# Optimization experiments

Measured on AMD Instinct MI355X. Metric: run time of the kernel, lower is better.

Reference implementation:

```python
import jax, jax.numpy as jnp
import numpy as np

HW = 128  # BEV heatmap size hardcoded in the module

def conv2d(x, w, b, pad):
    y = jax.lax.conv_general_dilated(x, w, (1, 1), [(pad, pad), (pad, pad)],
                                     dimension_numbers=('NCHW', 'OIHW', 'NCHW'))
    return y + b[None, :, None, None]

def setup_inputs() -> dict:
    key = jax.random.key(0)
    ks = jax.random.split(key, 8)
    B, C, N = 4, 64, 4096
    middle_feat_lidar = jax.random.normal(ks[0], (B, C, HW, HW), dtype=jnp.float32)
    voxels_feat_radar = jax.random.normal(ks[1], (N, C), dtype=jnp.float32)
    rcoors = jax.random.randint(ks[2], (N, 4), 0, HW, dtype=jnp.int64)
    rcoors = rcoors.at[:, 0].set(rcoors[:, 0] % B)  # batch index in [0, B)
    rcs = jax.random.uniform(ks[3], (N,), dtype=jnp.float32) * 6.0
    gamma = jnp.array(1.0, dtype=jnp.float32)  # self.rcs_gamma
    # rcs_att: Conv2d(2, C, 1); compress: Conv2d(2C, C, 3, pad=1)
    att_w = jax.random.normal(ks[4], (C, 2, 1, 1), dtype=jnp.float32) * 0.5
    att_b = jnp.zeros((C,), dtype=jnp.float32)
    comp_w = jax.random.normal(ks[5], (C, 2 * C, 3, 3), dtype=jnp.float32) * (1.0 / np.sqrt(2 * C * 9))
    comp_b = jnp.zeros((C,), dtype=jnp.float32)
    return {"middle_feat_lidar": middle_feat_lidar, "voxels_feat_radar": voxels_feat_radar,
            "rcoors": rcoors, "batch_size": B, "rcs": rcs, "gamma": gamma,
            "att_w": att_w, "att_b": att_b, "comp_w": comp_w, "comp_b": comp_b}

def _draw_maps(rcoors, rcs, gamma, batch_size):
    # Vectorized CenterPoint-style gaussian scatter-max over all N points.
    true_rcs = jax.nn.relu(rcs)                      # (N,)
    r = jnp.floor(gamma * true_rcs + 1.0)            # int() truncation; radius >= 1
    sigma = (2.0 * r + 1.0) / 6.0                    # sigma = diameter / 6
    b = rcoors[:, 0]
    y = rcoors[:, 2].astype(jnp.float32)
    x = rcoors[:, 3].astype(jnp.float32)
    grid = jnp.arange(HW, dtype=jnp.float32)
    dy = grid[None, :] - y[:, None]                  # (N, HW) rows
    dx = grid[None, :] - x[:, None]                  # (N, HW) cols
    g = jnp.exp(-(dy[:, :, None] ** 2 + dx[:, None, :] ** 2)
                / (2.0 * sigma[:, None, None] ** 2))  # (N, HW, HW)
    eps = jnp.finfo(jnp.float32).eps
    g = jnp.where(g < eps, 0.0, g)                   # gaussian_2d eps cutoff (max is 1 at center)
    # truncate gaussian to its (2r+1) box, as the slicing in draw_heatmap_gaussian does
    box = (jnp.abs(dy[:, :, None]) <= r[:, None, None]) & (jnp.abs(dx[:, None, :]) <= r[:, None, None])
    g = jnp.where(box, g, 0.0)
    heatmap = jnp.maximum(jax.ops.segment_max(g, b, num_segments=batch_size), 0.0)          # (B,HW,HW)
    heatmap_feat = jnp.maximum(
        jax.ops.segment_max(g * true_rcs[:, None, None], b, num_segments=batch_size), 0.0)  # (B,HW,HW)
    return heatmap, heatmap_feat

def reference(middle_feat_lidar, voxels_feat_radar, rcoors, batch_size, rcs,
              gamma, att_w, att_b, comp_w, comp_b):
    heatmap, heatmap_feat = _draw_maps(rcoors, rcs, gamma, batch_size)
    hm2 = jnp.stack([heatmap, heatmap_feat], axis=1)        # (B,2,HW,HW)
    rcs_features = conv2d(hm2, att_w, att_b, pad=0)          # 1x1 conv
    fused = jnp.concatenate([middle_feat_lidar, rcs_features], axis=1)
    return conv2d(fused, comp_w, comp_b, pad=1)              # 3x3 conv
```

## Files before the change

kernel.cpp:

```cpp
#include <hip/hip_runtime.h>
#include <math.h>

#define HW 128
#define CCH 64

typedef unsigned short u16;
typedef __attribute__((ext_vector_type(8))) short bf16x8;
typedef __attribute__((ext_vector_type(4))) float f32x4;

static __device__ __forceinline__ u16 f2bf(float x) {
    unsigned int u = __float_as_uint(x);
    unsigned int r = (u + 0x7FFFu + ((u >> 16) & 1u)) >> 16;
    return (u16)r;
}

__global__ void prep_kernel(const float* __restrict__ comp_w,
                            const float* __restrict__ att_w,
                            const float* __restrict__ att_b,
                            const int* __restrict__ rcoors,
                            const float* __restrict__ rcs,
                            const float* __restrict__ gamma_p,
                            float* __restrict__ Hm, float* __restrict__ Fm,
                            u16* __restrict__ Wp, int N, int B) {
    __shared__ float part[27][8];
    __shared__ float W3[27];
    int blk = blockIdx.x, tid = threadIdx.x;
    if (blk < 64) {
        int co = blk;
        if (tid < 216) {
            int d = tid >> 3, s = tid & 7;
            int t = d / 3, a = d - t * 3;
            float sum = 0.f;
#pragma unroll
            for (int q = 0; q < 8; ++q) {
                int c2 = s * 8 + q;
                float ww = comp_w[((size_t)co * 128 + 64 + c2) * 9 + t];
                float av = (a == 0) ? att_w[c2 * 2 + 0]
                         : (a == 1) ? att_w[c2 * 2 + 1]
                                    : att_b[c2];
                sum = fmaf(ww, av, sum);
            }
            part[d][s] = sum;
        }
        __syncthreads();
        if (tid < 27) {
            float s = 0.f;
#pragma unroll
            for (int q = 0; q < 8; ++q) s += part[tid][q];
            W3[tid] = s;
        }
        __syncthreads();
        for (int k = tid; k < 672; k += 256) {
            int oct = k >> 3, j = k & 7;
            u16 v = 0;
            if (oct < 81) {
                int t = oct / 9, o = oct - t * 9;
                int ci = o * 8 + j;
                float w = 0.0f;
                if (ci < 64)      w = comp_w[((size_t)co * 128 + ci) * 9 + t];
                else if (ci < 67) w = W3[t * 3 + (ci - 64)];
                v = f2bf(w);
            }
            Wp[co * 672 + k] = v;
        }
    } else {
        int n = blk - 64;
        if (n >= N) return;
        int b  = rcoors[n * 4 + 0];
        int yi = rcoors[n * 4 + 2];
        int xi = rcoors[n * 4 + 3];
        if ((unsigned)b >= (unsigned)B) return;
        float tr = fmaxf(rcs[n], 0.0f);
        float r = floorf(gamma_p[0] * tr + 1.0f);
        float sigma = (2.0f * r + 1.0f) * (1.0f / 6.0f);
        float inv2s2 = 1.0f / (2.0f * sigma * sigma);
        int R = (int)r;
        int W = 2 * R + 1;
        int tot = W * W;
        for (int cell = tid; cell < tot; cell += 256) {
            int cy = cell / W;
            int cx = cell - cy * W;
            int iy = yi - R + cy;
            int ix = xi - R + cx;
            if ((unsigned)iy >= HW || (unsigned)ix >= HW) continue;
            float dy = (float)(iy - yi), dx = (float)(ix - xi);
            float g = expf(-(dy * dy + dx * dx) * inv2s2);
            if (g < 1.1920929e-7f) continue;
            int idx = (b * HW + iy) * HW + ix;
            atomicMax((int*)&Hm[idx], __float_as_int(g));
            float gf = g * tr;
            if (gf > 0.0f) atomicMax((int*)&Fm[idx], __float_as_int(gf));
        }
    }
}

__global__ __launch_bounds__(256)
void conv_kernel(const float* __restrict__ middle,
                 const float* __restrict__ Hm, const float* __restrict__ Fm,
                 const u16* __restrict__ Wp, const float* __restrict__ comp_b,
                 float* __restrict__ out) {
    const int bx = blockIdx.x, by = blockIdx.y, b = blockIdx.z;
    const int tid = threadIdx.x;
    const int wave = tid >> 6, lane = tid & 63;
    const int col = lane & 15, quad = lane >> 4;
    const int i0 = by * 16 - 1, j0 = bx * 16 - 1;

    __shared__ u16 Xs[18 * 18 * 72];

    {
        const float* midB = middle + (size_t)b * CCH * HW * HW;
        const float* HmB = Hm + b * HW * HW;
        const float* FmB = Fm + b * HW * HW;
#pragma unroll 1
        for (int k0 = 0; k0 < 12; k0 += 6) {
            float rb[6][8];
#pragma unroll
            for (int q = 0; q < 6; ++q) {
                int u = tid + (k0 + q) * 256;
                int oct = u / 324, site = u - oct * 324;
                int rr = site / 18, cc = site - rr * 18;
                int gi = i0 + rr, gj = j0 + cc;
                bool in = (u < 2916) && ((unsigned)gi < HW) && ((unsigned)gj < HW);
                int off = in ? (gi * HW + gj) : 0;
                if (oct < 8) {
                    const float* p = midB + (size_t)(in ? oct : 0) * 8 * HW * HW + off;
#pragma unroll
                    for (int j = 0; j < 8; ++j)
                        rb[q][j] = p[(size_t)j * HW * HW];
                } else {
                    rb[q][0] = HmB[off];
                    rb[q][1] = FmB[off];
                }
            }
#pragma unroll
            for (int q = 0; q < 6; ++q) {
                int u = tid + (k0 + q) * 256;
                if (u >= 2916) continue;
                int oct = u / 324, site = u - oct * 324;
                int rr = site / 18, cc = site - rr * 18;
                int gi = i0 + rr, gj = j0 + cc;
                bool in = ((unsigned)gi < HW) && ((unsigned)gj < HW);
                union { u16 h[8]; uint4 v; } pk;
                pk.v = make_uint4(0u, 0u, 0u, 0u);
                if (in) {
                    if (oct < 8) {
#pragma unroll
                        for (int j = 0; j < 8; ++j) pk.h[j] = f2bf(rb[q][j]);
                    } else {
                        pk.h[0] = f2bf(rb[q][0]);
                        pk.h[1] = f2bf(rb[q][1]);
                        pk.h[2] = 0x3F80u;
                    }
                }
                *(uint4*)(Xs + site * 72 + oct * 8) = pk.v;
            }
        }
    }
    __syncthreads();

    f32x4 acc[4][4];
#pragma unroll
    for (int m = 0; m < 4; ++m)
#pragma unroll
        for (int n = 0; n < 4; ++n) acc[m][n] = (f32x4){0.f, 0.f, 0.f, 0.f};

#pragma unroll
    for (int c = 0; c < 21; ++c) {
        bf16x8 af[4];
#pragma unroll
        for (int m = 0; m < 4; ++m)
            af[m] = *(const bf16x8*)(Wp + (m * 16 + col) * 672 + c * 32 + quad * 8);

        int oct = c * 4 + quad;
        if (oct > 80) oct = 80;
        int t  = oct / 9;
        int o  = oct - t * 9;
        int dy = t / 3, dx = t - dy * 3;
        const u16* Bb = Xs + ((wave * 4 + dy) * 18 + (col + dx)) * 72 + o * 8;

        bf16x8 bfr[4];
#pragma unroll
        for (int n = 0; n < 4; ++n)
            bfr[n] = *(const bf16x8*)(Bb + n * (18 * 72));

#pragma unroll
        for (int m = 0; m < 4; ++m)
#pragma unroll
            for (int n = 0; n < 4; ++n)
                acc[m][n] = __builtin_amdgcn_mfma_f32_16x16x32_bf16(af[m], bfr[n], acc[m][n], 0, 0, 0);
    }

#pragma unroll
    for (int m = 0; m < 4; ++m) {
        int co0 = m * 16 + quad * 4;
#pragma unroll
        for (int n = 0; n < 4; ++n) {
            int i = by * 16 + wave * 4 + n;
            int j = bx * 16 + col;
            float* o0 = out + (((size_t)(b * 64 + co0) * HW + i) * HW + j);
#pragma unroll
            for (int r = 0; r < 4; ++r)
                o0[(size_t)r * HW * HW] = acc[m][n][r] + comp_b[co0 + r];
        }
    }
}

extern "C" void kernel_launch(void* const* d_in, const int* in_sizes, int n_in,
                              void* d_out, int out_size, void* d_ws, size_t ws_size,
                              hipStream_t stream) {
    const float* middle  = (const float*)d_in[0];
    const int*   rcoors  = (const int*)d_in[2];
    const float* rcs     = (const float*)d_in[4];
    const float* gamma   = (const float*)d_in[5];
    const float* att_w   = (const float*)d_in[6];
    const float* att_b   = (const float*)d_in[7];
    const float* comp_w  = (const float*)d_in[8];
    const float* comp_b  = (const float*)d_in[9];
    float* out = (float*)d_out;

    int B = in_sizes[0] / (CCH * HW * HW);
    int N = in_sizes[4];

    float* Hm = (float*)d_ws;
    float* Fm = Hm + (size_t)B * HW * HW;
    u16*   Wp = (u16*)(Fm + (size_t)B * HW * HW);

    prep_kernel<<<dim3(64 + N), 256, 0, stream>>>(comp_w, att_w, att_b,
                                                  rcoors, rcs, gamma,
                                                  Hm, Fm, Wp, N, B);
    conv_kernel<<<dim3(8, 8, B), 256, 0, stream>>>(middle, Hm, Fm, Wp, comp_b, out);
}
```

Baseline: 104.9 us.

## Shrink conv tile to 4x16 and split output channels across waves

The conv kernel now has each block compute a 4-row by 16-column output tile instead of 16x16, and each wave handles 16 output channels instead of 4 rows. The grid grows from 256 to 1024 blocks, which fills more CUs on the large GPU, and shared memory per block drops sharply, allowing higher occupancy. The cost is more halo reloading: 6 input rows are staged per 4 output rows instead of 18 per 16, which raises global read traffic on the 64-channel input. Per-wave MFMA register use also drops.

```diff
diff --git a/kernel.cpp b/kernel.cpp
--- a/kernel.cpp
+++ b/kernel.cpp
@@ -103,104 +103,90 @@
     const int tid = threadIdx.x;
     const int wave = tid >> 6, lane = tid & 63;
     const int col = lane & 15, quad = lane >> 4;
-    const int i0 = by * 16 - 1, j0 = bx * 16 - 1;
-
-    __shared__ u16 Xs[18 * 18 * 72];
+    const int i0 = by * 4 - 1, j0 = bx * 16 - 1;
+
+    __shared__ u16 Xs[6 * 18 * 72];
 
     {
         const float* midB = middle + (size_t)b * CCH * HW * HW;
         const float* HmB = Hm + b * HW * HW;
         const float* FmB = Fm + b * HW * HW;
-#pragma unroll 1
-        for (int k0 = 0; k0 < 12; k0 += 6) {
-            float rb[6][8];
-#pragma unroll
-            for (int q = 0; q < 6; ++q) {
-                int u = tid + (k0 + q) * 256;
-                int oct = u / 324, site = u - oct * 324;
-                int rr = site / 18, cc = site - rr * 18;
-                int gi = i0 + rr, gj = j0 + cc;
-                bool in = (u < 2916) && ((unsigned)gi < HW) && ((unsigned)gj < HW);
-                int off = in ? (gi * HW + gj) : 0;
+        float rb[4][8];
+#pragma unroll
+        for (int q = 0; q < 4; ++q) {
+            int u = tid + q * 256;
+            int oct = u / 108, site = u - oct * 108;
+            int rr = site / 18, cc = site - rr * 18;
+            int gi = i0 + rr, gj = j0 + cc;
+            bool in = (u < 972) && ((unsigned)gi < HW) && ((unsigned)gj < HW);
+            int off = in ? (gi * HW + gj) : 0;
+            if (oct < 8) {
+                const float* p = midB + (size_t)(in ? oct : 0) * 8 * HW * HW + off;
+#pragma unroll
+                for (int j = 0; j < 8; ++j)
+                    rb[q][j] = p[(size_t)j * HW * HW];
+            } else {
+                rb[q][0] = HmB[off];
+                rb[q][1] = FmB[off];
+            }
+        }
+#pragma unroll
+        for (int q = 0; q < 4; ++q) {
+            int u = tid + q * 256;
+            if (u >= 972) continue;
+            int oct = u / 108, site = u - oct * 108;
+            int rr = site / 18, cc = site - rr * 18;
+            int gi = i0 + rr, gj = j0 + cc;
+            bool in = ((unsigned)gi < HW) && ((unsigned)gj < HW);
+            union { u16 h[8]; uint4 v; } pk;
+            pk.v = make_uint4(0u, 0u, 0u, 0u);
+            if (in) {
                 if (oct < 8) {
-                    const float* p = midB + (size_t)(in ? oct : 0) * 8 * HW * HW + off;
-#pragma unroll
-                    for (int j = 0; j < 8; ++j)
-                        rb[q][j] = p[(size_t)j * HW * HW];
+#pragma unroll
+                    for (int j = 0; j < 8; ++j) pk.h[j] = f2bf(rb[q][j]);
                 } else {
-                    rb[q][0] = HmB[off];
-                    rb[q][1] = FmB[off];
+                    pk.h[0] = f2bf(rb[q][0]);
+                    pk.h[1] = f2bf(rb[q][1]);
+                    pk.h[2] = 0x3F80u;
                 }
             }
-#pragma unroll
-            for (int q = 0; q < 6; ++q) {
-                int u = tid + (k0 + q) * 256;
-                if (u >= 2916) continue;
-                int oct = u / 324, site = u - oct * 324;
-                int rr = site / 18, cc = site - rr * 18;
-                int gi = i0 + rr, gj = j0 + cc;
-                bool in = ((unsigned)gi < HW) && ((unsigned)gj < HW);
-                union { u16 h[8]; uint4 v; } pk;
-                pk.v = make_uint4(0u, 0u, 0u, 0u);
-                if (in) {
-                    if (oct < 8) {
-#pragma unroll
-                        for (int j = 0; j < 8; ++j) pk.h[j] = f2bf(rb[q][j]);
-                    } else {
-                        pk.h[0] = f2bf(rb[q][0]);
-                        pk.h[1] = f2bf(rb[q][1]);
-                        pk.h[2] = 0x3F80u;
-                    }
-                }
-                *(uint4*)(Xs + site * 72 + oct * 8) = pk.v;
-            }
+            *(uint4*)(Xs + site * 72 + oct * 8) = pk.v;
         }
     }
     __syncthreads();
 
-    f32x4 acc[4][4];
-#pragma unroll
-    for (int m = 0; m < 4; ++m)
-#pragma unroll
-        for (int n = 0; n < 4; ++n) acc[m][n] = (f32x4){0.f, 0.f, 0.f, 0.f};
+    f32x4 acc[4];
+#pragma unroll
+    for (int n = 0; n < 4; ++n) acc[n] = (f32x4){0.f, 0.f, 0.f, 0.f};
 
 #pragma unroll
     for (int c = 0; c < 21; ++c) {
-        bf16x8 af[4];
-#pragma unroll
-        for (int m = 0; m < 4; ++m)
-            af[m] = *(const bf16x8*)(Wp + (m * 16 + col) * 672 + c * 32 + quad * 8);
+        bf16x8 af = *(const bf16x8*)(Wp + (wave * 16 + col) * 672 + c * 32 + quad * 8);
 
         int oct = c * 4 + quad;
         if (oct > 80) oct = 80;
         int t  = oct / 9;
         int o  = oct - t * 9;
         int dy = t / 3, dx = t - dy * 3;
-        const u16* Bb = Xs + ((wave * 4 + dy) * 18 + (col + dx)) * 72 + o * 8;
-
-        bf16x8 bfr[4];
-#pragma unroll
-        for (int n = 0; n < 4; ++n)
-            bfr[n] = *(const bf16x8*)(Bb + n * (18 * 72));
-
-#pragma unroll
-        for (int m = 0; m < 4; ++m)
-#pragma unroll
-            for (int n = 0; n < 4; ++n)
-                acc[m][n] = __builtin_amdgcn_mfma_f32_16x16x32_bf16(af[m], bfr[n], acc[m][n], 0, 0, 0);
-    }
-
-#pragma unroll
-    for (int m = 0; m < 4; ++m) {
-        int co0 = m * 16 + quad * 4;
+        const u16* Bb = Xs + (dy * 18 + (col + dx)) * 72 + o * 8;
+
 #pragma unroll
         for (int n = 0; n < 4; ++n) {
-            int i = by * 16 + wave * 4 + n;
-            int j = bx * 16 + col;
+            bf16x8 bfr = *(const bf16x8*)(Bb + n * (18 * 72));
+            acc[n] = __builtin_amdgcn_mfma_f32_16x16x32_bf16(af, bfr, acc[n], 0, 0, 0);
+        }
+    }
+
+    {
+        int co0 = wave * 16 + quad * 4;
+        int j = bx * 16 + col;
+#pragma unroll
+        for (int n = 0; n < 4; ++n) {
+            int i = by * 4 + n;
             float* o0 = out + (((size_t)(b * 64 + co0) * HW + i) * HW + j);
 #pragma unroll
             for (int r = 0; r < 4; ++r)
-                o0[(size_t)r * HW * HW] = acc[m][n][r] + comp_b[co0 + r];
+                o0[(size_t)r * HW * HW] = acc[n][r] + comp_b[co0 + r];
         }
     }
 }
@@ -228,5 +214,5 @@
     prep_kernel<<<dim3(64 + N), 256, 0, stream>>>(comp_w, att_w, att_b,
                                                   rcoors, rcs, gamma,
                                                   Hm, Fm, Wp, N, B);
-    conv_kernel<<<dim3(8, 8, B), 256, 0, stream>>>(middle, Hm, Fm, Wp, comp_b, out);
-}
+    conv_kernel<<<dim3(8, 32, B), 256, 0, stream>>>(middle, Hm, Fm, Wp, comp_b, out);
+}
```

After: 102.1 us. -2.7%, faster.
